# Kernel tuning notes

Measured on AMD Instinct MI355X. Metric: run time of the kernel, lower is better.

Reference implementation:

```python
import jax, jax.numpy as jnp
import numpy as np

B, CDD, L, T, H, NH = 16, 10, 64, 128, 768, 12
DH = H // NH          # head dim = 64
S = CDD * L + T       # full sequence = 768 (640 candidate tokens + 128 terms)


def setup_inputs() -> dict:
    key = jax.random.key(0)
    ks = jax.random.split(key, 7)
    w = 0.02
    return {
        "hidden_states": jax.random.normal(ks[0], (B, S, H), jnp.float32),
        "Wq": jax.random.normal(ks[1], (H, H), jnp.float32) * w,
        "bq": jax.random.normal(ks[2], (H,), jnp.float32) * w,
        "Wk": jax.random.normal(ks[3], (H, H), jnp.float32) * w,
        "bk": jax.random.normal(ks[4], (H,), jnp.float32) * w,
        "Wv": jax.random.normal(ks[5], (H, H), jnp.float32) * w,
        "bv": jax.random.normal(ks[6], (H,), jnp.float32) * w,
    }


def _one_pass_mask(dtype):
    # block-diagonal over candidates + dense global columns for terms
    block = jnp.kron(jnp.eye(CDD, dtype=dtype), jnp.ones((L, L), dtype=dtype))  # [CDD*L, CDD*L]
    return jnp.concatenate([block, jnp.ones((CDD * L, T), dtype=dtype)], axis=-1)  # [CDD*L, S]


def reference(hidden_states, Wq, bq, Wk, bk, Wv, bv):
    def split_heads(x):  # [B, s, H] -> [B, NH, s, DH]
        return x.reshape(B, -1, NH, DH).transpose(0, 2, 1, 3)

    attn_field = hidden_states[:, :-T]                     # [B, CDD*L, H] queries only
    q = split_heads(attn_field @ Wq.T + bq)                # [B, NH, CDD*L, DH]
    k = split_heads(hidden_states @ Wk.T + bk)             # [B, NH, S, DH]
    v = split_heads(hidden_states @ Wv.T + bv)             # [B, NH, S, DH]

    mask = _one_pass_mask(q.dtype)                         # [CDD*L, S]
    scale = 1.0 / np.sqrt(DH).astype(np.float32)
    # NOTE: original multiplies scores by the mask (masked entries become 0, not -inf)
    scores = jnp.einsum('bhqd,bhkd->bhqk', q, k) * scale * mask
    probs = jax.nn.softmax(scores, axis=-1)                # [B, NH, CDD*L, S]

    ctx = jnp.einsum('bhqk,bhkd->bhqd', probs, v)          # [B, NH, CDD*L, DH]
    ctx = jnp.concatenate([ctx, v[:, :, -T:]], axis=2)     # append term values untouched
    return ctx.transpose(0, 2, 1, 3).reshape(B, S, H)
```

## Files before the change

kernel.cpp:

```cpp
#include <hip/hip_runtime.h>

constexpr int Bb  = 16;
constexpr int CDD = 10;
constexpr int Lc  = 64;
constexpr int T   = 128;
constexpr int H   = 768;
constexpr int NH  = 12;
constexpr int DH  = 64;
constexpr int S   = 768;
constexpr int SQ  = 640;
constexpr int MROWS = Bb * S;

typedef __attribute__((ext_vector_type(8))) short bf16x8;
typedef __attribute__((ext_vector_type(4))) short bf16x4;
typedef __attribute__((ext_vector_type(4))) float f32x4;

__device__ inline unsigned short f2bf(float f) {
  unsigned u = __float_as_uint(f);
  u += 0x7fff + ((u >> 16) & 1);
  return (unsigned short)(u >> 16);
}
__device__ inline float bf2f(unsigned short h) {
  return __uint_as_float(((unsigned)h) << 16);
}

__device__ inline void gld_lds16(const void* g, void* l) {
  __builtin_amdgcn_global_load_lds(
      (const __attribute__((address_space(1))) void*)g,
      (__attribute__((address_space(3))) void*)l, 16, 0, 0);
}

__device__ inline bf16x8 ld_b64x2(const unsigned short* p) {
  union { bf16x8 v; bf16x4 h[2]; } u;
  u.h[0] = *(const bf16x4*)p;
  u.h[1] = *(const bf16x4*)(p + 4);
  return u.v;
}

constexpr int NX4 = MROWS * H / 4;
constexpr int NW4 = H * H / 4;
__global__ void convert_all(const float* __restrict__ X,
                            const float* __restrict__ Wq,
                            const float* __restrict__ Wk,
                            const float* __restrict__ Wv,
                            unsigned short* __restrict__ Xb,
                            unsigned short* __restrict__ Wb) {
  int i = blockIdx.x * blockDim.x + threadIdx.x;
  const int stride = gridDim.x * blockDim.x;
  const int total = NX4 + 3 * NW4;
  for (; i < total; i += stride) {
    const float* src;
    unsigned short* dst;
    int off;
    if (i < NX4) {
      src = X; dst = Xb; off = i;
    } else {
      int k = i - NX4;
      int w = k / NW4;
      off = k - w * NW4;
      src = (w == 0) ? Wq : (w == 1) ? Wk : Wv;
      dst = Wb + (size_t)w * H * H;
    }
    float4 v = ((const float4*)src)[off];
    ushort4 o;
    o.x = f2bf(v.x); o.y = f2bf(v.y); o.z = f2bf(v.z); o.w = f2bf(v.w);
    ((ushort4*)dst)[off] = o;
  }
}

__launch_bounds__(256, 4)
__global__ void qkv_gemm(const unsigned short* __restrict__ Xb,
                         const unsigned short* __restrict__ Wb,
                         const float* __restrict__ bq, const float* __restrict__ bk,
                         const float* __restrict__ bv,
                         unsigned short* __restrict__ Qb, unsigned short* __restrict__ Kb,
                         unsigned short* __restrict__ Vb,
                         float* __restrict__ out) {
  const int z = blockIdx.z;
  const unsigned short* W = Wb + (size_t)z * H * H;
  const float* bias = (z == 0) ? bq : (z == 1) ? bk : bv;
  unsigned short* Y = (z == 0) ? Qb : (z == 1) ? Kb : Vb;

  const int i0 = blockIdx.x * 128;
  const int j0 = blockIdx.y * 128;
  const int tid = threadIdx.x;
  const int wave = tid >> 6, lane = tid & 63;
  const int wr = wave >> 1, wc = wave & 1;
  const int col = lane & 15, quad = lane >> 4;

  __shared__ unsigned short As[128 * 32];
  __shared__ unsigned short Bs[128 * 32];

  f32x4 acc[4][4];
#pragma unroll
  for (int i = 0; i < 4; i++)
#pragma unroll
    for (int j = 0; j < 4; j++) acc[i][j] = (f32x4){0.f, 0.f, 0.f, 0.f};

  const int rowA0 = tid >> 2, csA0 = tid & 3;
  const int rowA1 = (tid + 256) >> 2, csA1 = tid & 3;
  const int gcA0 = csA0 ^ ((rowA0 >> 1) & 3);
  const int gcA1 = csA1 ^ ((rowA1 >> 1) & 3);

  for (int kt = 0; kt < 24; kt++) {
    const int k0 = kt * 32;
    gld_lds16(Xb + (size_t)(i0 + rowA0) * H + k0 + gcA0 * 8, &As[tid * 8]);
    gld_lds16(Xb + (size_t)(i0 + rowA1) * H + k0 + gcA1 * 8, &As[(tid + 256) * 8]);
    gld_lds16(W  + (size_t)(j0 + rowA0) * H + k0 + gcA0 * 8, &Bs[tid * 8]);
    gld_lds16(W  + (size_t)(j0 + rowA1) * H + k0 + gcA1 * 8, &Bs[(tid + 256) * 8]);
    __builtin_amdgcn_s_waitcnt(0);
    __syncthreads();

    bf16x8 a[4], b[4];
#pragma unroll
    for (int mt = 0; mt < 4; mt++) {
      int r = wr * 64 + mt * 16 + col;
      a[mt] = *(const bf16x8*)&As[r * 32 + ((quad ^ ((r >> 1) & 3)) * 8)];
    }
#pragma unroll
    for (int nt = 0; nt < 4; nt++) {
      int r = wc * 64 + nt * 16 + col;
      b[nt] = *(const bf16x8*)&Bs[r * 32 + ((quad ^ ((r >> 1) & 3)) * 8)];
    }
#pragma unroll
    for (int mt = 0; mt < 4; mt++)
#pragma unroll
      for (int nt = 0; nt < 4; nt++)
        acc[mt][nt] = __builtin_amdgcn_mfma_f32_16x16x32_bf16(a[mt], b[nt], acc[mt][nt], 0, 0, 0);
    __syncthreads();
  }

#pragma unroll
  for (int mt = 0; mt < 4; mt++) {
#pragma unroll
    for (int nt = 0; nt < 4; nt++) {
      const int j = j0 + wc * 64 + nt * 16 + col;
      const float bj = bias[j];
#pragma unroll
      for (int r = 0; r < 4; r++) {
        const int i = i0 + wr * 64 + mt * 16 + quad * 4 + r;
        const float v = acc[mt][nt][r] + bj;
        Y[(size_t)i * H + j] = f2bf(v);
        if (z == 2) {
          int s = i - (i / S) * S;
          if (s >= SQ) out[(size_t)i * H + j] = v;
        }
      }
    }
  }
}

__global__ void vtot_partial(const unsigned short* __restrict__ Vb,
                             float* __restrict__ part) {
  const int b = blockIdx.x;
  const int j = blockIdx.y * 256 + threadIdx.x;
  const int rs = blockIdx.z;
  const unsigned short* p = Vb + (size_t)(b * S + rs * 96) * H + j;
  float s = 0.f;
#pragma unroll 8
  for (int r = 0; r < 96; r++) s += bf2f(p[(size_t)r * H]);
  part[(size_t)(b * 8 + rs) * H + j] = s;
}

__launch_bounds__(256, 2)
__global__ void attn_kernel(const unsigned short* __restrict__ Qb,
                            const unsigned short* __restrict__ Kb,
                            const unsigned short* __restrict__ Vb,
                            const float* __restrict__ part,
                            float* __restrict__ out) {
  const int bid = blockIdx.x;
  const int c = bid % CDD;
  const int h = (bid / CDD) % NH;
  const int b = bid / (CDD * NH);
  const int tid = threadIdx.x;
  const int wave = tid >> 6, lane = tid & 63;
  const int col = lane & 15, quad = lane >> 4;

  __shared__ __align__(16) char smem[59136];
  unsigned short* Qs = (unsigned short*)smem;
  unsigned short* Ks = (unsigned short*)(smem + 8192);
  unsigned short* Ps = (unsigned short*)smem;
  unsigned short* Vt = (unsigned short*)(smem + 32768);
  float* red   = (float*)(smem + 57856);
  float* vcorr = (float*)(smem + 58880);

  const size_t rowQ0 = (size_t)(b * S + c * 64) * H + h * DH;

  {
    int s0 = tid, s1 = tid + 256;
    int r0 = s0 >> 3, g0 = (s0 & 7) ^ (r0 & 7);
    int r1 = s1 >> 3, g1 = (s1 & 7) ^ (r1 & 7);
    gld_lds16(Qb + rowQ0 + (size_t)r0 * H + g0 * 8, &Qs[s0 * 8]);
    gld_lds16(Qb + rowQ0 + (size_t)r1 * H + g1 * 8, &Qs[s1 * 8]);
  }
#pragma unroll
  for (int j = 0; j < 6; j++) {
    int s = tid + 256 * j;
    int key = s >> 3;
    int gkey = (key < 64) ? (c * 64 + key) : (576 + key);
    int gc = (s & 7) ^ (key & 7);
    gld_lds16(Kb + (size_t)(b * S + gkey) * H + h * DH + gc * 8, &Ks[s * 8]);
  }
#pragma unroll
  for (int j = 0; j < 6; j++) {
    int s = tid + 256 * j;
    int key = s >> 3;
    int f0 = (s & 7) * 8;
    int gkey = (key < 64) ? (c * 64 + key) : (576 + key);
    union { int4 i4; unsigned short u[8]; } uv;
    uv.i4 = *(const int4*)(Vb + (size_t)(b * S + gkey) * H + h * DH + f0);
#pragma unroll
    for (int i = 0; i < 8; i++) Vt[(f0 + i) * 196 + key] = uv.u[i];
  }
  __builtin_amdgcn_s_waitcnt(0);
  __syncthreads();

  {
    int d = tid & 63, p = tid >> 6;
    float sum = 0.f;
    for (int k = p * 48; k < p * 48 + 48; k++) sum += bf2f(Vt[d * 196 + k]);
    red[tid] = sum;
  }
  __syncthreads();
  if (tid < 64) {
    float tot = 0.f;
#pragma unroll
    for (int rs = 0; rs < 8; rs++) tot += part[(size_t)(b * 8 + rs) * H + h * DH + tid];
    vcorr[tid] = tot - (red[tid] + red[64 + tid] + red[128 + tid] + red[192 + tid]);
  }

  f32x4 sc[12];
#pragma unroll
  for (int n = 0; n < 12; n++) sc[n] = (f32x4){0.f, 0.f, 0.f, 0.f};
  {
    const int rq = wave * 16 + col;
    bf16x8 a0 = *(const bf16x8*)&Qs[rq * 64 + ((quad ^ (rq & 7)) * 8)];
    bf16x8 a1 = *(const bf16x8*)&Qs[rq * 64 + (((4 + quad) ^ (rq & 7)) * 8)];
#pragma unroll
    for (int n = 0; n < 12; n++) {
      const int rk = n * 16 + col;
      bf16x8 b0 = *(const bf16x8*)&Ks[rk * 64 + ((quad ^ (rk & 7)) * 8)];
      bf16x8 b1 = *(const bf16x8*)&Ks[rk * 64 + (((4 + quad) ^ (rk & 7)) * 8)];
      sc[n] = __builtin_amdgcn_mfma_f32_16x16x32_bf16(a0, b0, sc[n], 0, 0, 0);
      sc[n] = __builtin_amdgcn_mfma_f32_16x16x32_bf16(a1, b1, sc[n], 0, 0, 0);
    }
  }

  float em[4], zin[4];
  {
    const float scale = 0.125f;
#pragma unroll
    for (int r = 0; r < 4; r++) {
      float mx = sc[0][r];
#pragma unroll
      for (int n = 1; n < 12; n++) mx = fmaxf(mx, sc[n][r]);
#pragma unroll
      for (int msk = 1; msk <= 8; msk <<= 1) mx = fmaxf(mx, __shfl_xor(mx, msk, 64));
      const float mrow = fmaxf(mx * scale, 0.f);
      float rs = 0.f;
#pragma unroll
      for (int n = 0; n < 12; n++) {
        float p = __expf(sc[n][r] * scale - mrow);
        sc[n][r] = p;
        rs += p;
      }
#pragma unroll
      for (int msk = 1; msk <= 8; msk <<= 1) rs += __shfl_xor(rs, msk, 64);
      const float e = __expf(-mrow);
      em[r] = e;
      zin[r] = 1.f / (rs + 576.f * e);
    }
  }
  __syncthreads();

#pragma unroll
  for (int n = 0; n < 12; n++)
#pragma unroll
    for (int r = 0; r < 4; r++)
      Ps[(wave * 16 + quad * 4 + r) * 196 + n * 16 + col] = f2bf(sc[n][r]);
  __syncthreads();

  f32x4 o[4];
#pragma unroll
  for (int n2 = 0; n2 < 4; n2++) o[n2] = (f32x4){0.f, 0.f, 0.f, 0.f};
#pragma unroll
  for (int ks = 0; ks < 6; ks++) {
    bf16x8 a = ld_b64x2(&Ps[(wave * 16 + col) * 196 + ks * 32 + quad * 8]);
#pragma unroll
    for (int n2 = 0; n2 < 4; n2++) {
      bf16x8 bvv = ld_b64x2(&Vt[(n2 * 16 + col) * 196 + ks * 32 + quad * 8]);
      o[n2] = __builtin_amdgcn_mfma_f32_16x16x32_bf16(a, bvv, o[n2], 0, 0, 0);
    }
  }

#pragma unroll
  for (int n2 = 0; n2 < 4; n2++) {
    const int d = n2 * 16 + col;
    const float vc = vcorr[d];
#pragma unroll
    for (int r = 0; r < 4; r++) {
      const int m = wave * 16 + quad * 4 + r;
      const float val = (o[n2][r] + em[r] * vc) * zin[r];
      out[(size_t)(b * S + c * 64 + m) * H + h * DH + d] = val;
    }
  }
}

extern "C" void kernel_launch(void* const* d_in, const int* in_sizes, int n_in,
                              void* d_out, int out_size, void* d_ws, size_t ws_size,
                              hipStream_t stream) {
  const float* X  = (const float*)d_in[0];
  const float* Wq = (const float*)d_in[1];
  const float* bq = (const float*)d_in[2];
  const float* Wk = (const float*)d_in[3];
  const float* bk = (const float*)d_in[4];
  const float* Wv = (const float*)d_in[5];
  const float* bv = (const float*)d_in[6];
  float* out = (float*)d_out;

  char* ws = (char*)d_ws;
  unsigned short* Xb   = (unsigned short*)ws;
  unsigned short* Wb   = (unsigned short*)(ws + 18874368);
  unsigned short* Qb   = (unsigned short*)(ws + 22413312);
  unsigned short* Kb   = (unsigned short*)(ws + 41287680);
  unsigned short* Vb   = (unsigned short*)(ws + 60162048);
  float*          part = (float*)(ws + 79036416);

  convert_all<<<2048, 256, 0, stream>>>(X, Wq, Wk, Wv, Xb, Wb);
  qkv_gemm<<<dim3(96, 6, 3), 256, 0, stream>>>(Xb, Wb, bq, bk, bv, Qb, Kb, Vb, out);
  vtot_partial<<<dim3(16, 3, 8), 256, 0, stream>>>(Vb, part);
  attn_kernel<<<1920, 256, 0, stream>>>(Qb, Kb, Vb, part, out);
}
```

Measured before the change: 193.4 us.

## Widen GEMM K-tile, skip unused Q rows, fuse V column sums into GEMM epilogue

The QKV GEMM now stages a 64-wide K slice per iteration instead of 32, which halves the number of barrier and load rounds and uses an 8-way XOR swizzle. Q-projection blocks that cover only term rows (the last 128 of each batch) now exit early, since those queries are never used. The separate vtot_partial kernel is removed: the V-projection epilogue reduces per-column sums with shuffles and atomically adds them into a per-batch buffer, which is zeroed by a memset. This adds float atomics, whose nondeterministic summation order slightly changes rounding, and doubles LDS per block, which may lower occupancy.

Result: faster. 181.6 us (-6.1%).

```diff
diff --git a/kernel.cpp b/kernel.cpp
--- a/kernel.cpp
+++ b/kernel.cpp
@@ -61,7 +61,7 @@
       src = (w == 0) ? Wq : (w == 1) ? Wk : Wv;
       dst = Wb + (size_t)w * H * H;
     }
-    float4 v = ((const float4*)src)[off];
+    float4 v = ((const float4*)src)[i < NX4 ? off : off];
     ushort4 o;
     o.x = f2bf(v.x); o.y = f2bf(v.y); o.z = f2bf(v.z); o.w = f2bf(v.w);
     ((ushort4*)dst)[off] = o;
@@ -75,8 +75,10 @@
                          const float* __restrict__ bv,
                          unsigned short* __restrict__ Qb, unsigned short* __restrict__ Kb,
                          unsigned short* __restrict__ Vb,
+                         float* __restrict__ part,
                          float* __restrict__ out) {
   const int z = blockIdx.z;
+  if (z == 0 && (blockIdx.x % 6) == 5) return;
   const unsigned short* W = Wb + (size_t)z * H * H;
   const float* bias = (z == 0) ? bq : (z == 1) ? bk : bv;
   unsigned short* Y = (z == 0) ? Qb : (z == 1) ? Kb : Vb;
@@ -88,8 +90,8 @@
   const int wr = wave >> 1, wc = wave & 1;
   const int col = lane & 15, quad = lane >> 4;
 
-  __shared__ unsigned short As[128 * 32];
-  __shared__ unsigned short Bs[128 * 32];
+  __shared__ unsigned short As[128 * 64];
+  __shared__ unsigned short Bs[128 * 64];
 
   f32x4 acc[4][4];
 #pragma unroll
@@ -97,39 +99,48 @@
 #pragma unroll
     for (int j = 0; j < 4; j++) acc[i][j] = (f32x4){0.f, 0.f, 0.f, 0.f};
 
-  const int rowA0 = tid >> 2, csA0 = tid & 3;
-  const int rowA1 = (tid + 256) >> 2, csA1 = tid & 3;
-  const int gcA0 = csA0 ^ ((rowA0 >> 1) & 3);
-  const int gcA1 = csA1 ^ ((rowA1 >> 1) & 3);
-
-  for (int kt = 0; kt < 24; kt++) {
-    const int k0 = kt * 32;
-    gld_lds16(Xb + (size_t)(i0 + rowA0) * H + k0 + gcA0 * 8, &As[tid * 8]);
-    gld_lds16(Xb + (size_t)(i0 + rowA1) * H + k0 + gcA1 * 8, &As[(tid + 256) * 8]);
-    gld_lds16(W  + (size_t)(j0 + rowA0) * H + k0 + gcA0 * 8, &Bs[tid * 8]);
-    gld_lds16(W  + (size_t)(j0 + rowA1) * H + k0 + gcA1 * 8, &Bs[(tid + 256) * 8]);
+  int rS[4], gcS[4];
+#pragma unroll
+  for (int i = 0; i < 4; i++) {
+    int s = tid + 256 * i;
+    rS[i] = s >> 3;
+    gcS[i] = (s & 7) ^ (rS[i] & 7);
+  }
+
+  for (int kt = 0; kt < 12; kt++) {
+    const int k0 = kt * 64;
+#pragma unroll
+    for (int i = 0; i < 4; i++)
+      gld_lds16(Xb + (size_t)(i0 + rS[i]) * H + k0 + gcS[i] * 8, &As[(tid + 256 * i) * 8]);
+#pragma unroll
+    for (int i = 0; i < 4; i++)
+      gld_lds16(W + (size_t)(j0 + rS[i]) * H + k0 + gcS[i] * 8, &Bs[(tid + 256 * i) * 8]);
     __builtin_amdgcn_s_waitcnt(0);
     __syncthreads();
 
-    bf16x8 a[4], b[4];
-#pragma unroll
-    for (int mt = 0; mt < 4; mt++) {
-      int r = wr * 64 + mt * 16 + col;
-      a[mt] = *(const bf16x8*)&As[r * 32 + ((quad ^ ((r >> 1) & 3)) * 8)];
-    }
-#pragma unroll
-    for (int nt = 0; nt < 4; nt++) {
-      int r = wc * 64 + nt * 16 + col;
-      b[nt] = *(const bf16x8*)&Bs[r * 32 + ((quad ^ ((r >> 1) & 3)) * 8)];
-    }
-#pragma unroll
-    for (int mt = 0; mt < 4; mt++)
-#pragma unroll
-      for (int nt = 0; nt < 4; nt++)
-        acc[mt][nt] = __builtin_amdgcn_mfma_f32_16x16x32_bf16(a[mt], b[nt], acc[mt][nt], 0, 0, 0);
+#pragma unroll
+    for (int h = 0; h < 2; h++) {
+      bf16x8 a[4], b[4];
+#pragma unroll
+      for (int mt = 0; mt < 4; mt++) {
+        int r = wr * 64 + mt * 16 + col;
+        a[mt] = *(const bf16x8*)&As[r * 64 + (((h * 4 + quad) ^ (r & 7)) * 8)];
+      }
+#pragma unroll
+      for (int nt = 0; nt < 4; nt++) {
+        int r = wc * 64 + nt * 16 + col;
+        b[nt] = *(const bf16x8*)&Bs[r * 64 + (((h * 4 + quad) ^ (r & 7)) * 8)];
+      }
+#pragma unroll
+      for (int mt = 0; mt < 4; mt++)
+#pragma unroll
+        for (int nt = 0; nt < 4; nt++)
+          acc[mt][nt] = __builtin_amdgcn_mfma_f32_16x16x32_bf16(a[mt], b[nt], acc[mt][nt], 0, 0, 0);
+    }
     __syncthreads();
   }
 
+  float colsum[4] = {0.f, 0.f, 0.f, 0.f};
 #pragma unroll
   for (int mt = 0; mt < 4; mt++) {
 #pragma unroll
@@ -142,24 +153,26 @@
         const float v = acc[mt][nt][r] + bj;
         Y[(size_t)i * H + j] = f2bf(v);
         if (z == 2) {
+          colsum[nt] += v;
           int s = i - (i / S) * S;
           if (s >= SQ) out[(size_t)i * H + j] = v;
         }
       }
     }
   }
-}
-
-__global__ void vtot_partial(const unsigned short* __restrict__ Vb,
-                             float* __restrict__ part) {
-  const int b = blockIdx.x;
-  const int j = blockIdx.y * 256 + threadIdx.x;
-  const int rs = blockIdx.z;
-  const unsigned short* p = Vb + (size_t)(b * S + rs * 96) * H + j;
-  float s = 0.f;
-#pragma unroll 8
-  for (int r = 0; r < 96; r++) s += bf2f(p[(size_t)r * H]);
-  part[(size_t)(b * 8 + rs) * H + j] = s;
+  if (z == 2) {
+    const int b = blockIdx.x / 6;
+#pragma unroll
+    for (int nt = 0; nt < 4; nt++) {
+      float s = colsum[nt];
+      s += __shfl_xor(s, 16, 64);
+      s += __shfl_xor(s, 32, 64);
+      if (quad == 0) {
+        const int j = j0 + wc * 64 + nt * 16 + col;
+        atomicAdd(&part[b * H + j], s);
+      }
+    }
+  }
 }
 
 __launch_bounds__(256, 2)
@@ -223,9 +236,7 @@
   }
   __syncthreads();
   if (tid < 64) {
-    float tot = 0.f;
-#pragma unroll
-    for (int rs = 0; rs < 8; rs++) tot += part[(size_t)(b * 8 + rs) * H + h * DH + tid];
+    float tot = part[b * H + h * DH + tid];
     vcorr[tid] = tot - (red[tid] + red[64 + tid] + red[128 + tid] + red[192 + tid]);
   }
 
@@ -326,8 +337,8 @@
   unsigned short* Vb   = (unsigned short*)(ws + 60162048);
   float*          part = (float*)(ws + 79036416);
 
+  hipMemsetAsync(part, 0, Bb * H * sizeof(float), stream);
   convert_all<<<2048, 256, 0, stream>>>(X, Wq, Wk, Wv, Xb, Wb);
-  qkv_gemm<<<dim3(96, 6, 3), 256, 0, stream>>>(Xb, Wb, bq, bk, bv, Qb, Kb, Vb, out);
-  vtot_partial<<<dim3(16, 3, 8), 256, 0, stream>>>(Vb, part);
+  qkv_gemm<<<dim3(96, 6, 3), 256, 0, stream>>>(Xb, Wb, bq, bk, bv, Qb, Kb, Vb, part, out);
   attn_kernel<<<1920, 256, 0, stream>>>(Qb, Kb, Vb, part, out);
 }
```
